# Performance work log

Hardware: AMD Instinct MI355X
Metric: run time of the kernel (lower is better)

## Reference

```python
import jax, jax.numpy as jnp
import numpy as np

WS = (8, 8)          # window size (Wh, Ww)
SS = (4, 4)          # shift size
DIM = 512
HEADS = 16
HD = DIM // HEADS    # 32
D1 = (HD // 2) // 2  # 8
D2 = (HD // 2) - D1  # 8
EPS = 1e-5
B, H, W = 4, 128, 128
HIDDEN = int(DIM * 4.0)  # 2048 (swiglu -> fc1 out = 2*HIDDEN)


def _layer_norm(x, g, b):
    m = jnp.mean(x, -1, keepdims=True)
    v = jnp.mean((x - m) ** 2, -1, keepdims=True)
    return (x - m) * jax.lax.rsqrt(v + EPS) * g + b


def _rope_tables():
    wh, ww = WS
    inv1 = 10000.0 ** (-(jnp.arange(D1, dtype=jnp.float32) / D1))
    inv2 = 10000.0 ** (-(jnp.arange(D2, dtype=jnp.float32) / D2))
    rows = jnp.arange(wh, dtype=jnp.float32)[:, None] * inv1  # (wh, D1)
    cols = jnp.arange(ww, dtype=jnp.float32)[:, None] * inv2  # (ww, D2)
    sin1 = jnp.broadcast_to(jnp.sin(rows)[:, None, :], (wh, ww, D1))
    cos1 = jnp.broadcast_to(jnp.cos(rows)[:, None, :], (wh, ww, D1))
    sin2 = jnp.broadcast_to(jnp.sin(cols)[None, :, :], (wh, ww, D2))
    cos2 = jnp.broadcast_to(jnp.cos(cols)[None, :, :], (wh, ww, D2))
    return sin1, cos1, sin2, cos2


def _rope2d(t, tabs):
    # t: (B_*heads, wh, ww, HD)
    sin1, cos1, sin2, cos2 = tabs
    x11 = t[..., :D1]
    x21 = t[..., D1:D1 + D2]
    x12 = t[..., D1 + D2:D1 + D2 + D1]
    x22 = t[..., D1 + D2 + D1:]
    return jnp.concatenate([
        x11 * cos1 - x12 * sin1,
        x21 * cos2 - x22 * sin2,
        x12 * cos1 + x11 * sin1,
        x22 * cos2 + x21 * sin2,
    ], axis=-1)


def _swin_mask():
    wh, ww = WS
    img = np.zeros((H, W), dtype=np.float32)
    cnt = 0
    for hs in (slice(0, -wh), slice(-wh, -SS[0]), slice(-SS[0], None)):
        for ws in (slice(0, -ww), slice(-ww, -SS[1]), slice(-SS[1], None)):
            img[hs, ws] = cnt
            cnt += 1
    mw = img.reshape(H // wh, wh, W // ww, ww).transpose(0, 2, 1, 3).reshape(-1, wh * ww)
    diff = mw[:, None, :] - mw[:, :, None]
    return jnp.asarray(np.where(diff != 0, -100.0, 0.0).astype(np.float32))


def setup_inputs() -> dict:
    key = jax.random.key(0)
    ks = jax.random.split(key, 14)
    s = 0.02
    return {
        "x": jax.random.normal(ks[0], (B, H, W, DIM), jnp.float32),
        "attn_mask": _swin_mask(),
        "norm1_g": jnp.ones((DIM,), jnp.float32),
        "norm1_b": jnp.zeros((DIM,), jnp.float32),
        "qkv_w": jax.random.normal(ks[1], (3 * DIM, DIM), jnp.float32) * s,
        "qkv_b": jnp.zeros((3 * DIM,), jnp.float32),
        "proj_w": jax.random.normal(ks[2], (DIM, DIM), jnp.float32) * s,
        "proj_b": jnp.zeros((DIM,), jnp.float32),
        "norm2_g": jnp.ones((DIM,), jnp.float32),
        "norm2_b": jnp.zeros((DIM,), jnp.float32),
        "fc1_w": jax.random.normal(ks[3], (2 * HIDDEN, DIM), jnp.float32) * s,
        "fc1_b": jnp.zeros((2 * HIDDEN,), jnp.float32),
        "fc2_w": jax.random.normal(ks[4], (DIM, HIDDEN), jnp.float32) * s,
        "fc2_b": jnp.zeros((DIM,), jnp.float32),
    }


def reference(x, attn_mask, norm1_g, norm1_b, qkv_w, qkv_b, proj_w, proj_b,
              norm2_g, norm2_b, fc1_w, fc1_b, fc2_w, fc2_b):
    wh, ww = WS
    N = wh * ww
    nH, nW = H // wh, W // ww
    nWin = nH * nW
    B_ = B * nWin
    tabs = _rope_tables()

    shortcut = x
    xn = _layer_norm(x, norm1_g, norm1_b)
    # cyclic shift
    xs = jnp.roll(xn, (-SS[0], -SS[1]), axis=(1, 2))
    # window partition: (B,H,W,C) -> (B*nWin, N, C)
    xw = xs.reshape(B, nH, wh, nW, ww, DIM).transpose(0, 1, 3, 2, 4, 5).reshape(B_, N, DIM)

    qkv = xw @ qkv_w.T + qkv_b
    qkv = qkv.reshape(B_, N, 3, HEADS, HD).transpose(2, 0, 3, 1, 4)  # (3,B_,h,N,hd)
    q, k, v = qkv[0], qkv[1], qkv[2]
    # inline 2D RoPE on q,k per window
    q = _rope2d(q.reshape(-1, wh, ww, HD), tabs).reshape(B_, HEADS, N, HD)
    k = _rope2d(k.reshape(-1, wh, ww, HD), tabs).reshape(B_, HEADS, N, HD)

    scale = HD ** -0.5
    attn = jnp.einsum('bhnd,bhmd->bhnm', q * scale, k)
    attn = attn.reshape(B, nWin, HEADS, N, N) + attn_mask[None, :, None]
    attn = jax.nn.softmax(attn.reshape(B_, HEADS, N, N), axis=-1)

    out = jnp.einsum('bhnm,bhmd->bhnd', attn, v).transpose(0, 2, 1, 3).reshape(B_, N, DIM)
    out = out @ proj_w.T + proj_b
    # window reverse + reverse shift
    out = out.reshape(B, nH, nW, wh, ww, DIM).transpose(0, 1, 3, 2, 4, 5).reshape(B, H, W, DIM)
    out = jnp.roll(out, (SS[0], SS[1]), axis=(1, 2))

    x = shortcut + out
    # SwiGLU MLP
    y = _layer_norm(x, norm2_g, norm2_b)
    h = y @ fc1_w.T + fc1_b
    a, gate = jnp.split(h, 2, axis=-1)
    h = jax.nn.silu(gate) * a
    y = h @ fc2_w.T + fc2_b
    return x + y
```

## Files before the change

kernel.cpp:

```cpp
#include <hip/hip_runtime.h>
#include <stdint.h>

typedef __attribute__((ext_vector_type(8))) short bf16x8;
typedef __attribute__((ext_vector_type(4))) float f32x4;
typedef __attribute__((ext_vector_type(4))) int i32x4;
typedef unsigned short u16;

#define GLD_LDS16(g, l) __builtin_amdgcn_global_load_lds( \
    (const __attribute__((address_space(1))) void*)(g),   \
    (__attribute__((address_space(3))) void*)(l), 16, 0, 0)

#define PB() do { __builtin_amdgcn_sched_barrier(0); \
                  __builtin_amdgcn_s_barrier();      \
                  __builtin_amdgcn_sched_barrier(0); } while (0)

#define ACCI(d, a_, b_)  d = __builtin_amdgcn_mfma_i32_16x16x64_i8(a_, b_, d, 0, 0, 0)

#define INV_A (1.0f / 16384.0f)
#define INV_P (1.0f / 32768.0f)
#define INV_H (1.0f / 65536.0f)

__device__ __forceinline__ u16 f2bf(float f) {
  union { float f; uint32_t u; } a; a.f = f;
  uint32_t u = a.u;
  return (u16)((u + 0x7fffu + ((u >> 16) & 1u)) >> 16);
}
__device__ __forceinline__ float bf2f(u16 h) {
  union { uint32_t u; float f; } a; a.u = ((uint32_t)h) << 16;
  return a.f;
}
__device__ __forceinline__ uint32_t q8x4(float a, float b, float c, float d, float s) {
  int qa = (int)rintf(fminf(fmaxf(a * s, -127.f), 127.f));
  int qb = (int)rintf(fminf(fmaxf(b * s, -127.f), 127.f));
  int qc = (int)rintf(fminf(fmaxf(c * s, -127.f), 127.f));
  int qd = (int)rintf(fminf(fmaxf(d * s, -127.f), 127.f));
  return (qa & 255) | ((qb & 255) << 8) | ((qc & 255) << 16) | ((qd & 255) << 24);
}
__device__ __forceinline__ char q8(float v, float s) {
  return (char)(int)rintf(fminf(fmaxf(v * s, -127.f), 127.f));
}

__global__ __launch_bounds__(256) void ln1_wconv(const float* __restrict__ x,
    const float* __restrict__ gw, const float* __restrict__ bw, char* __restrict__ out,
    const float* __restrict__ qw, const float* __restrict__ pw,
    const float* __restrict__ f1w, const float* __restrict__ f2w,
    char* __restrict__ wb8) {
  int bx = blockIdx.x;
  if (bx >= 16384) {
    int i4 = (bx - 16384) * 1024 + threadIdx.x * 4;
    float w[4];
#pragma unroll
    for (int j = 0; j < 4; j++) {
      int idx = i4 + j;
      if (idx < 786432)        w[j] = qw[idx];
      else if (idx < 1048576)  w[j] = pw[idx - 786432];
      else if (idx < 3145728)  w[j] = f1w[idx - 1048576];
      else                     w[j] = f2w[idx - 3145728];
    }
    *(uint32_t*)(wb8 + i4) = q8x4(w[0], w[1], w[2], w[3], 1024.f);
    return;
  }
  int wid = threadIdx.x >> 6;
  int lane = threadIdx.x & 63;
  int m = (bx << 2) + wid;
  int n = m & 63;
  int bwin = m >> 6;
  int b = bwin >> 8;
  int wi = bwin & 255;
  int h = (((wi >> 4) << 3) + (n >> 3) + 4) & 127;
  int w = (((wi & 15) << 3) + (n & 7) + 4) & 127;
  const float* src = x + (((size_t)((b << 7) + h) << 7) + (size_t)w) * 512;
  int ch = lane << 3;
  float4 v0 = *(const float4*)(src + ch);
  float4 v1 = *(const float4*)(src + ch + 4);
  float vv[8] = {v0.x, v0.y, v0.z, v0.w, v1.x, v1.y, v1.z, v1.w};
  float s = 0.f, s2 = 0.f;
#pragma unroll
  for (int j = 0; j < 8; j++) { s += vv[j]; s2 += vv[j] * vv[j]; }
#pragma unroll
  for (int off = 32; off; off >>= 1) {
    s += __shfl_xor(s, off);
    s2 += __shfl_xor(s2, off);
  }
  float mean = s * (1.f / 512.f);
  float var = s2 * (1.f / 512.f) - mean * mean;
  float rstd = rsqrtf(var + 1e-5f);
  float y[8];
#pragma unroll
  for (int j = 0; j < 8; j++) y[j] = (vv[j] - mean) * rstd * gw[ch + j] + bw[ch + j];
  uint2 o;
  o.x = q8x4(y[0], y[1], y[2], y[3], 16.f);
  o.y = q8x4(y[4], y[5], y[6], y[7], 16.f);
  *(uint2*)(out + ((size_t)m << 9) + ch) = o;
}

__global__ __launch_bounds__(256) void ln2_q8(const u16* __restrict__ sb,
    const float* __restrict__ gw, const float* __restrict__ bw,
    char* __restrict__ out) {
  int wid = threadIdx.x >> 6;
  int lane = threadIdx.x & 63;
  int m = (blockIdx.x << 2) + wid;
  int ch = lane << 3;
  union { uint4 u; u16 hh[8]; } in;
  in.u = *(const uint4*)(sb + ((size_t)m << 9) + ch);
  float vv[8];
#pragma unroll
  for (int j = 0; j < 8; j++) vv[j] = bf2f(in.hh[j]);
  float s = 0.f, s2 = 0.f;
#pragma unroll
  for (int j = 0; j < 8; j++) { s += vv[j]; s2 += vv[j] * vv[j]; }
#pragma unroll
  for (int off = 32; off; off >>= 1) {
    s += __shfl_xor(s, off);
    s2 += __shfl_xor(s2, off);
  }
  float mean = s * (1.f / 512.f);
  float var = s2 * (1.f / 512.f) - mean * mean;
  float rstd = rsqrtf(var + 1e-5f);
  float y[8];
#pragma unroll
  for (int j = 0; j < 8; j++) y[j] = (vv[j] - mean) * rstd * gw[ch + j] + bw[ch + j];
  uint2 o;
  o.x = q8x4(y[0], y[1], y[2], y[3], 16.f);
  o.y = q8x4(y[4], y[5], y[6], y[7], 16.f);
  *(uint2*)(out + ((size_t)m << 9) + ch) = o;
}

template<int EPI, int K>
__global__ __launch_bounds__(512, 4) void gemm2i(
    const char* __restrict__ A, const char* __restrict__ Bw,
    const float* __restrict__ bias, void* __restrict__ outp,
    const float* __restrict__ resid, int NTN) {
  __shared__ __align__(16) char lds[2][3][8192];
  const int NT = K / 64;
  int bid = blockIdx.x;
  int nwg = gridDim.x;
  int wg = (bid & 7) * (nwg >> 3) + (bid >> 3);
  int mt = wg / NTN, nt = wg - mt * NTN;
  int m0 = mt << 7;
  int n0 = (EPI == 3) ? (nt << 7) : (nt << 8);

  int tid = threadIdx.x;
  int wid = tid >> 6, lane = tid & 63;
  int wm = wid >> 2, wn = wid & 3;
  int l15 = lane & 15, lhi = lane >> 4;

  int sr0 = tid >> 2;
  int sc = (tid & 3) ^ ((sr0 >> 1) & 3);
  const char* gA  = A  + (size_t)(m0 + sr0) * K + sc * 16;
  const char* gB0 = Bw + (size_t)(n0 + sr0) * K + sc * 16;
  const char* gB1 = (EPI == 3)
      ? (Bw + (size_t)(2048 + n0 + sr0) * K + sc * 16)
      : (Bw + (size_t)(n0 + 128 + sr0) * K + sc * 16);

  auto stage = [&](int slot, const char* gp, int t) {
    if (t >= NT) return;
    char* ld = &lds[t & 1][slot][0] + tid * 16;
    GLD_LDS16(gp + t * 64, ld);
  };

  int aoff[4], boff[2];
#pragma unroll
  for (int i = 0; i < 4; i++) {
    int r = wm * 64 + i * 16 + l15;
    aoff[i] = r * 64 + ((lhi ^ ((r >> 1) & 3)) << 4);
  }
#pragma unroll
  for (int j = 0; j < 2; j++) {
    int r = wn * 32 + j * 16 + l15;
    boff[j] = r * 64 + ((lhi ^ ((r >> 1) & 3)) << 4);
  }

  i32x4 acc[2][4][2] = {};
  i32x4 afr[4], b0r[2], b1r[2];

  stage(0, gA, 0); stage(1, gB0, 0); stage(2, gB1, 0);
  stage(0, gA, 1); stage(1, gB0, 1);
  asm volatile("s_waitcnt vmcnt(2)" ::: "memory");
  __builtin_amdgcn_sched_barrier(0);
  __builtin_amdgcn_s_barrier();
  __builtin_amdgcn_sched_barrier(0);

  for (int s = 0; s < NT; ++s) {
    const char* Ah  = &lds[s & 1][0][0];
    const char* B0h = &lds[s & 1][1][0];
    const char* B1h = &lds[s & 1][2][0];

#pragma unroll
    for (int i = 0; i < 4; i++) afr[i] = *(const i32x4*)&Ah[aoff[i]];
#pragma unroll
    for (int j = 0; j < 2; j++) b0r[j] = *(const i32x4*)&B0h[boff[j]];
    stage(2, gB1, s + 1);
    PB();
    __builtin_amdgcn_s_setprio(1);
#pragma unroll
    for (int i = 0; i < 4; i++)
#pragma unroll
      for (int j = 0; j < 2; j++) ACCI(acc[0][i][j], afr[i], b0r[j]);
    __builtin_amdgcn_s_setprio(0);
    PB();

#pragma unroll
    for (int j = 0; j < 2; j++) b1r[j] = *(const i32x4*)&B1h[boff[j]];
    stage(0, gA, s + 2);
    stage(1, gB0, s + 2);
    PB();
    __builtin_amdgcn_s_setprio(1);
#pragma unroll
    for (int i = 0; i < 4; i++)
#pragma unroll
      for (int j = 0; j < 2; j++) ACCI(acc[1][i][j], afr[i], b1r[j]);
    __builtin_amdgcn_s_setprio(0);
    if (s >= NT - 2) { asm volatile("s_waitcnt vmcnt(0)" ::: "memory"); }
    else             { asm volatile("s_waitcnt vmcnt(2)" ::: "memory"); }
    __builtin_amdgcn_sched_barrier(0);
    __builtin_amdgcn_s_barrier();
    __builtin_amdgcn_sched_barrier(0);
  }

#pragma unroll
  for (int i = 0; i < 4; i++) {
    int row = m0 + wm * 64 + i * 16 + lhi * 4;
    if (EPI == 0) {
      u16* out = (u16*)outp;
#pragma unroll
      for (int h = 0; h < 2; h++)
#pragma unroll
        for (int j = 0; j < 2; j++) {
          int colb = n0 + h * 128 + wn * 32 + j * 16;
          int col = colb + l15;
          int sh = colb >> 5;
          int d = (colb & 31) + l15;
          float bv = bias[col];
#pragma unroll
          for (int rg = 0; rg < 4; rg++)
            out[(size_t)sh * 2097152 + (size_t)(row + rg) * 32 + d] =
                f2bf((float)acc[h][i][j][rg] * INV_A + bv);
        }
    } else if (EPI == 1) {
      u16* sbw = (u16*)outp;
#pragma unroll
      for (int rg = 0; rg < 4; rg++) {
        int m = row + rg;
        int b = m >> 14, wi2 = (m >> 6) & 255, n = m & 63;
        int hh = (((wi2 >> 4) << 3) + (n >> 3) + 4) & 127;
        int w = (((wi2 & 15) << 3) + (n & 7) + 4) & 127;
        size_t pix = (((size_t)((b << 7) + hh) << 7) + (size_t)w) << 9;
#pragma unroll
        for (int h = 0; h < 2; h++)
#pragma unroll
          for (int j = 0; j < 2; j++) {
            int col = n0 + h * 128 + wn * 32 + j * 16 + l15;
            sbw[pix + col] = f2bf(resid[pix + col] +
                                  (float)acc[h][i][j][rg] * INV_P + bias[col]);
          }
      }
    } else if (EPI == 2) {
      float* out = (float*)outp;
      const u16* sbp = (const u16*)resid;
#pragma unroll
      for (int h = 0; h < 2; h++)
#pragma unroll
        for (int j = 0; j < 2; j++) {
          int col = n0 + h * 128 + wn * 32 + j * 16 + l15;
          float bv = bias[col];
#pragma unroll
          for (int rg = 0; rg < 4; rg++) {
            size_t idx = (size_t)(row + rg) * 512 + col;
            out[idx] = bf2f(sbp[idx]) + (float)acc[h][i][j][rg] * INV_H + bv;
          }
        }
    } else {
      char* out = (char*)outp;
#pragma unroll
      for (int j = 0; j < 2; j++) {
        int col = n0 + wn * 32 + j * 16 + l15;
        float ba_ = bias[col], bg_ = bias[col + 2048];
#pragma unroll
        for (int rg = 0; rg < 4; rg++) {
          float av = (float)acc[0][i][j][rg] * INV_A + ba_;
          float gv = (float)acc[1][i][j][rg] * INV_A + bg_;
          float sw = gv / (1.f + __expf(-gv));
          out[(size_t)(row + rg) * 2048 + col] = q8(sw * av, 64.f);
        }
      }
    }
  }
}

__global__ __launch_bounds__(256) void attn_mfma(
    const u16* __restrict__ qkv, char* __restrict__ out) {
  __shared__ __align__(16) char alds[4][15360];
  int tid = threadIdx.x;
  int wid = tid >> 6, lane = tid & 63;
  int bwin = blockIdx.x >> 2;
  int head = ((blockIdx.x & 3) << 2) + wid;
  int wi = bwin & 255;
  int wr = wi >> 4, wc = wi & 15;
  char* Wb = alds[wid];
  u16* Qr = (u16*)Wb;
  u16* Kr = (u16*)(Wb + 5120);
  u16* Vt = (u16*)(Wb + 10240);
  u16* PT = (u16*)Wb;
  int t = lane;
  int l15 = lane & 15, lhi = lane >> 4;
  size_t tok = (size_t)(bwin << 6) + t;
  const u16* qb = qkv + (size_t)head * 2097152 + tok * 32;
  union U { uint4 u; u16 s[8]; };
  U vq[4], vk[4], vv[4];
#pragma unroll
  for (int g = 0; g < 4; g++) {
    vq[g].u = *(const uint4*)(qb + (g << 3));
    vk[g].u = *(const uint4*)(qb + 33554432 + (g << 3));
    vv[g].u = *(const uint4*)(qb + 67108864 + (g << 3));
  }
  float q[32], k[32];
#pragma unroll
  for (int j = 0; j < 32; j++) {
    q[j] = bf2f(vq[j >> 3].s[j & 7]);
    k[j] = bf2f(vk[j >> 3].s[j & 7]);
  }
  int r = t >> 3, c = t & 7;
#pragma unroll
  for (int d = 0; d < 16; d++) {
    float pos = (d < 8) ? (float)r : (float)c;
    int dd = (d < 8) ? d : d - 8;
    float ang = pos * __expf(-(float)dd * 1.1512925465f);
    float sn, cs;
    __sincosf(ang, &sn, &cs);
    float q1 = q[d], q2 = q[d + 16];
    q[d] = q1 * cs - q2 * sn;  q[d + 16] = q2 * cs + q1 * sn;
    float k1 = k[d], k2 = k[d + 16];
    k[d] = k1 * cs - k2 * sn;  k[d + 16] = k2 * cs + k1 * sn;
  }
#pragma unroll
  for (int j = 0; j < 32; j++) q[j] *= 0.17677669529663687f;
#pragma unroll
  for (int sl = 0; sl < 4; sl++) {
    U tq, tk;
#pragma unroll
    for (int j = 0; j < 8; j++) { tq.s[j] = f2bf(q[sl * 8 + j]); tk.s[j] = f2bf(k[sl * 8 + j]); }
    *(uint4*)(Qr + t * 40 + sl * 8) = tq.u;
    *(uint4*)(Kr + t * 40 + sl * 8) = tk.u;
  }
#pragma unroll
  for (int j = 0; j < 32; j++) Vt[j * 72 + t] = vv[j >> 3].s[j & 7];
  bf16x8 kf[4], qf[4];
#pragma unroll
  for (int i = 0; i < 4; i++) {
    kf[i] = *(const bf16x8*)(Kr + (i * 16 + l15) * 40 + lhi * 8);
    qf[i] = *(const bf16x8*)(Qr + (i * 16 + l15) * 40 + lhi * 8);
  }
  f32x4 zz = {0.f, 0.f, 0.f, 0.f};
  f32x4 st[4][4];
#pragma unroll
  for (int mi = 0; mi < 4; mi++)
#pragma unroll
    for (int nj = 0; nj < 4; nj++)
      st[mi][nj] = __builtin_amdgcn_mfma_f32_16x16x32_bf16(kf[mi], qf[nj], zz, 0, 0, 0);
  if (wr == 15 || wc == 15) {
    int idh = (wr == 15) ? ((r >= 4) ? 2 : 1) : 0;
    int idw = (wc == 15) ? ((c >= 4) ? 2 : 1) : 0;
    int code = idh * 3 + idw;
    int cq[4], cm[4][4];
#pragma unroll
    for (int nj = 0; nj < 4; nj++) cq[nj] = __shfl(code, nj * 16 + l15);
#pragma unroll
    for (int mi = 0; mi < 4; mi++)
#pragma unroll
      for (int rg = 0; rg < 4; rg++) cm[mi][rg] = __shfl(code, mi * 16 + lhi * 4 + rg);
#pragma unroll
    for (int mi = 0; mi < 4; mi++)
#pragma unroll
      for (int nj = 0; nj < 4; nj++)
#pragma unroll
        for (int rg = 0; rg < 4; rg++)
          if (cm[mi][rg] != cq[nj]) st[mi][nj][rg] -= 100.f;
  }
  float inv_[4];
#pragma unroll
  for (int nj = 0; nj < 4; nj++) {
    float mx = -1e30f;
#pragma unroll
    for (int mi = 0; mi < 4; mi++)
#pragma unroll
      for (int rg = 0; rg < 4; rg++) mx = fmaxf(mx, st[mi][nj][rg]);
    mx = fmaxf(mx, __shfl_xor(mx, 16));
    mx = fmaxf(mx, __shfl_xor(mx, 32));
    float sum = 0.f;
#pragma unroll
    for (int mi = 0; mi < 4; mi++)
#pragma unroll
      for (int rg = 0; rg < 4; rg++) {
        float p = __expf(st[mi][nj][rg] - mx);
        st[mi][nj][rg] = p;
        sum += p;
      }
    sum += __shfl_xor(sum, 16);
    sum += __shfl_xor(sum, 32);
    inv_[nj] = 1.f / sum;
  }
#pragma unroll
  for (int mi = 0; mi < 4; mi++)
#pragma unroll
    for (int nj = 0; nj < 4; nj++) {
      uint32_t lo, hi;
      asm("v_cvt_pk_bf16_f32 %0, %1, %2" : "=v"(lo) : "v"(st[mi][nj][0]), "v"(st[mi][nj][1]));
      asm("v_cvt_pk_bf16_f32 %0, %1, %2" : "=v"(hi) : "v"(st[mi][nj][2]), "v"(st[mi][nj][3]));
      uint2 pr; pr.x = lo; pr.y = hi;
      *(uint2*)(PT + (nj * 16 + l15) * 72 + mi * 16 + lhi * 4) = pr;
    }
  bf16x8 vf[2][2], pf[4][2];
#pragma unroll
  for (int i = 0; i < 2; i++)
#pragma unroll
    for (int kc = 0; kc < 2; kc++)
      vf[i][kc] = *(const bf16x8*)(Vt + (i * 16 + l15) * 72 + kc * 32 + lhi * 8);
#pragma unroll
  for (int nj = 0; nj < 4; nj++)
#pragma unroll
    for (int kc = 0; kc < 2; kc++)
      pf[nj][kc] = *(const bf16x8*)(PT + (nj * 16 + l15) * 72 + kc * 32 + lhi * 8);
  char* Ot = Wb;
#pragma unroll
  for (int i = 0; i < 2; i++)
#pragma unroll
    for (int nj = 0; nj < 4; nj++) {
      f32x4 o = __builtin_amdgcn_mfma_f32_16x16x32_bf16(vf[i][0], pf[nj][0], zz, 0, 0, 0);
      o = __builtin_amdgcn_mfma_f32_16x16x32_bf16(vf[i][1], pf[nj][1], o, 0, 0, 0);
      float iv32 = inv_[nj] * 32.f;
      uint32_t pk = q8x4(o[0] * iv32, o[1] * iv32, o[2] * iv32, o[3] * iv32, 1.f);
      *(uint32_t*)(Ot + (nj * 16 + l15) * 40 + i * 16 + lhi * 4) = pk;
    }
#pragma unroll
  for (int g = 0; g < 4; g++) {
    int tl = g * 16 + (lane >> 2);
    int ch_ = (lane & 3) << 3;
    uint2 v = *(const uint2*)(Ot + tl * 40 + ch_);
    *(uint2*)(out + (size_t)((bwin << 6) + tl) * 512 + (head << 5) + ch_) = v;
  }
}

extern "C" void kernel_launch(void* const* d_in, const int* in_sizes, int n_in,
                              void* d_out, int out_size, void* d_ws, size_t ws_size,
                              hipStream_t stream) {
  (void)in_sizes; (void)n_in; (void)out_size; (void)ws_size;
  const float* x      = (const float*)d_in[0];
  const float* n1g    = (const float*)d_in[2];
  const float* n1b    = (const float*)d_in[3];
  const float* qkv_w  = (const float*)d_in[4];
  const float* qkv_b  = (const float*)d_in[5];
  const float* proj_w = (const float*)d_in[6];
  const float* proj_b = (const float*)d_in[7];
  const float* n2g    = (const float*)d_in[8];
  const float* n2b    = (const float*)d_in[9];
  const float* fc1_w  = (const float*)d_in[10];
  const float* fc1_b  = (const float*)d_in[11];
  const float* fc2_w  = (const float*)d_in[12];
  const float* fc2_b  = (const float*)d_in[13];

  const size_t MB = 1048576ULL;
  char* ws = (char*)d_ws;
  char* wb8  = ws;
  char* wq8  = wb8;
  char* wp8  = wb8 + 786432;
  char* wf18 = wb8 + 1048576;
  char* wf28 = wb8 + 3145728;
  char* xw8  = ws + 8 * MB;
  char* attn8 = xw8;
  u16*  qkvb = (u16*)(ws + 72 * MB);
  char* hb8  = ws + 8 * MB;
  u16*  sb   = (u16*)(ws + 264 * MB);
  char* yb8  = ws + 328 * MB;

  ln1_wconv<<<20480, 256, 0, stream>>>(x, n1g, n1b, xw8,
                                       qkv_w, proj_w, fc1_w, fc2_w, wb8);
  gemm2i<0, 512><<<3072, 512, 0, stream>>>(xw8, wq8, qkv_b, qkvb, nullptr, 6);
  attn_mfma<<<4096, 256, 0, stream>>>(qkvb, attn8);
  gemm2i<1, 512><<<1024, 512, 0, stream>>>(attn8, wp8, proj_b, sb, x, 2);
  ln2_q8<<<16384, 256, 0, stream>>>(sb, n2g, n2b, yb8);
  gemm2i<3, 512><<<8192, 512, 0, stream>>>(yb8, wf18, fc1_b, hb8, nullptr, 16);
  gemm2i<2, 2048><<<1024, 512, 0, stream>>>(hb8, wf28, fc2_b, d_out,
                                            (const float*)sb, 2);
}
```

Baseline: 564.7 us.

## Fuse projection GEMM with residual add and LayerNorm2 into one kernel

Replaces the separate projection GEMM (with residual epilogue) and the standalone ln2_q8 kernel with a single proj_ln2 kernel. Each workgroup computes a full 128x512 row tile, so it can do the row statistics for LayerNorm in its epilogue. Partial sums are reduced with lane shuffles and then through LDS across waves. It then writes both the bf16 residual sum and the int8-quantized normalized output. This removes a kernel launch and a full re-read of the bf16 intermediate, at the cost of a larger per-block tile, one block per CU, and byte-granular scattered stores.

```diff
diff --git a/kernel.cpp b/kernel.cpp
--- a/kernel.cpp
+++ b/kernel.cpp
@@ -94,38 +94,6 @@
   *(uint2*)(out + ((size_t)m << 9) + ch) = o;
 }
 
-__global__ __launch_bounds__(256) void ln2_q8(const u16* __restrict__ sb,
-    const float* __restrict__ gw, const float* __restrict__ bw,
-    char* __restrict__ out) {
-  int wid = threadIdx.x >> 6;
-  int lane = threadIdx.x & 63;
-  int m = (blockIdx.x << 2) + wid;
-  int ch = lane << 3;
-  union { uint4 u; u16 hh[8]; } in;
-  in.u = *(const uint4*)(sb + ((size_t)m << 9) + ch);
-  float vv[8];
-#pragma unroll
-  for (int j = 0; j < 8; j++) vv[j] = bf2f(in.hh[j]);
-  float s = 0.f, s2 = 0.f;
-#pragma unroll
-  for (int j = 0; j < 8; j++) { s += vv[j]; s2 += vv[j] * vv[j]; }
-#pragma unroll
-  for (int off = 32; off; off >>= 1) {
-    s += __shfl_xor(s, off);
-    s2 += __shfl_xor(s2, off);
-  }
-  float mean = s * (1.f / 512.f);
-  float var = s2 * (1.f / 512.f) - mean * mean;
-  float rstd = rsqrtf(var + 1e-5f);
-  float y[8];
-#pragma unroll
-  for (int j = 0; j < 8; j++) y[j] = (vv[j] - mean) * rstd * gw[ch + j] + bw[ch + j];
-  uint2 o;
-  o.x = q8x4(y[0], y[1], y[2], y[3], 16.f);
-  o.y = q8x4(y[4], y[5], y[6], y[7], 16.f);
-  *(uint2*)(out + ((size_t)m << 9) + ch) = o;
-}
-
 template<int EPI, int K>
 __global__ __launch_bounds__(512, 4) void gemm2i(
     const char* __restrict__ A, const char* __restrict__ Bw,
@@ -237,24 +205,6 @@
             out[(size_t)sh * 2097152 + (size_t)(row + rg) * 32 + d] =
                 f2bf((float)acc[h][i][j][rg] * INV_A + bv);
         }
-    } else if (EPI == 1) {
-      u16* sbw = (u16*)outp;
-#pragma unroll
-      for (int rg = 0; rg < 4; rg++) {
-        int m = row + rg;
-        int b = m >> 14, wi2 = (m >> 6) & 255, n = m & 63;
-        int hh = (((wi2 >> 4) << 3) + (n >> 3) + 4) & 127;
-        int w = (((wi2 & 15) << 3) + (n & 7) + 4) & 127;
-        size_t pix = (((size_t)((b << 7) + hh) << 7) + (size_t)w) << 9;
-#pragma unroll
-        for (int h = 0; h < 2; h++)
-#pragma unroll
-          for (int j = 0; j < 2; j++) {
-            int col = n0 + h * 128 + wn * 32 + j * 16 + l15;
-            sbw[pix + col] = f2bf(resid[pix + col] +
-                                  (float)acc[h][i][j][rg] * INV_P + bias[col]);
-          }
-      }
     } else if (EPI == 2) {
       float* out = (float*)outp;
       const u16* sbp = (const u16*)resid;
@@ -286,6 +236,172 @@
       }
     }
   }
+}
+
+__global__ __launch_bounds__(512, 1) void proj_ln2(
+    const char* __restrict__ A, const char* __restrict__ Bw,
+    const float* __restrict__ pbias, const float* __restrict__ g2,
+    const float* __restrict__ b2, const float* __restrict__ xres,
+    u16* __restrict__ sbw, char* __restrict__ yb8) {
+  __shared__ __align__(16) char lds[2][40960];
+  const int K = 512, NT = 8;
+  int bid = blockIdx.x;
+  int nwg = gridDim.x;
+  int wg = (bid & 7) * (nwg >> 3) + (bid >> 3);
+  int m0 = wg << 7;
+
+  int tid = threadIdx.x;
+  int wid = tid >> 6, lane = tid & 63;
+  int wm = wid >> 2, wn = wid & 3;
+  int l15 = lane & 15, lhi = lane >> 4;
+
+  int sr0 = tid >> 2;
+  int sc = (tid & 3) ^ ((sr0 >> 1) & 3);
+  const char* gA = A + (size_t)(m0 + sr0) * K + sc * 16;
+  const char* gB[4];
+#pragma unroll
+  for (int q = 0; q < 4; q++)
+    gB[q] = Bw + (size_t)(q * 128 + sr0) * K + sc * 16;
+
+  auto stageA = [&](int t) {
+    if (t >= NT) return;
+    GLD_LDS16(gA + t * 64, &lds[t & 1][0] + tid * 16);
+  };
+  auto stageB = [&](int q, int t) {
+    if (t >= NT) return;
+    GLD_LDS16(gB[q] + t * 64, &lds[t & 1][8192 + q * 8192] + tid * 16);
+  };
+
+  int aoff[4], boff[8];
+#pragma unroll
+  for (int i = 0; i < 4; i++) {
+    int r = wm * 64 + i * 16 + l15;
+    aoff[i] = r * 64 + ((lhi ^ ((r >> 1) & 3)) << 4);
+  }
+#pragma unroll
+  for (int j = 0; j < 8; j++) {
+    int r = wn * 128 + j * 16 + l15;
+    boff[j] = 8192 + r * 64 + ((lhi ^ ((r >> 1) & 3)) << 4);
+  }
+
+  i32x4 acc[4][8] = {};
+  i32x4 afr[4], br[4];
+
+  stageA(0); stageB(0, 0); stageB(1, 0); stageB(2, 0); stageB(3, 0);
+  stageA(1);
+  asm volatile("s_waitcnt vmcnt(1)" ::: "memory");
+  __builtin_amdgcn_sched_barrier(0);
+  __builtin_amdgcn_s_barrier();
+  __builtin_amdgcn_sched_barrier(0);
+
+  for (int s = 0; s < NT; ++s) {
+    const char* Lh = &lds[s & 1][0];
+
+#pragma unroll
+    for (int i = 0; i < 4; i++) afr[i] = *(const i32x4*)&Lh[aoff[i]];
+#pragma unroll
+    for (int j = 0; j < 4; j++) br[j] = *(const i32x4*)&Lh[boff[j]];
+    stageB(0, s + 1); stageB(1, s + 1); stageB(2, s + 1); stageB(3, s + 1);
+    PB();
+    __builtin_amdgcn_s_setprio(1);
+#pragma unroll
+    for (int i = 0; i < 4; i++)
+#pragma unroll
+      for (int j = 0; j < 4; j++) ACCI(acc[i][j], afr[i], br[j]);
+    __builtin_amdgcn_s_setprio(0);
+    PB();
+
+#pragma unroll
+    for (int j = 0; j < 4; j++) br[j] = *(const i32x4*)&Lh[boff[4 + j]];
+    stageA(s + 2);
+    PB();
+    __builtin_amdgcn_s_setprio(1);
+#pragma unroll
+    for (int i = 0; i < 4; i++)
+#pragma unroll
+      for (int j = 0; j < 4; j++) ACCI(acc[i][4 + j], afr[i], br[j]);
+    __builtin_amdgcn_s_setprio(0);
+    if (s >= NT - 2) { asm volatile("s_waitcnt vmcnt(0)" ::: "memory"); }
+    else             { asm volatile("s_waitcnt vmcnt(1)" ::: "memory"); }
+    __builtin_amdgcn_sched_barrier(0);
+    __builtin_amdgcn_s_barrier();
+    __builtin_amdgcn_sched_barrier(0);
+  }
+
+  float pb_[8], gv_[8], bv_[8];
+#pragma unroll
+  for (int j = 0; j < 8; j++) {
+    int col = wn * 128 + j * 16 + l15;
+    pb_[j] = pbias[col];
+    gv_[j] = g2[col];
+    bv_[j] = b2[col];
+  }
+  size_t pix[4][4];
+  float s1[4][4], s2_[4][4];
+#pragma unroll
+  for (int i = 0; i < 4; i++)
+#pragma unroll
+    for (int rg = 0; rg < 4; rg++) {
+      int m = m0 + wm * 64 + i * 16 + lhi * 4 + rg;
+      int b = m >> 14, wi2 = (m >> 6) & 255, n = m & 63;
+      int hh = (((wi2 >> 4) << 3) + (n >> 3) + 4) & 127;
+      int w = (((wi2 & 15) << 3) + (n & 7) + 4) & 127;
+      pix[i][rg] = (((size_t)((b << 7) + hh) << 7) + (size_t)w) << 9;
+      float a1 = 0.f, a2 = 0.f;
+#pragma unroll
+      for (int j = 0; j < 8; j++) {
+        int col = wn * 128 + j * 16 + l15;
+        float sv = xres[pix[i][rg] + col] + (float)acc[i][j][rg] * INV_P + pb_[j];
+        sbw[pix[i][rg] + col] = f2bf(sv);
+        acc[i][j][rg] = __float_as_int(sv);
+        a1 += sv; a2 += sv * sv;
+      }
+      s1[i][rg] = a1; s2_[i][rg] = a2;
+    }
+#pragma unroll
+  for (int i = 0; i < 4; i++)
+#pragma unroll
+    for (int rg = 0; rg < 4; rg++) {
+#pragma unroll
+      for (int off = 1; off < 16; off <<= 1) {
+        s1[i][rg] += __shfl_xor(s1[i][rg], off);
+        s2_[i][rg] += __shfl_xor(s2_[i][rg], off);
+      }
+    }
+  float* st = (float*)lds;
+  __syncthreads();
+  if (l15 == 0) {
+#pragma unroll
+    for (int i = 0; i < 4; i++)
+#pragma unroll
+      for (int rg = 0; rg < 4; rg++) {
+        int lrow = wm * 64 + i * 16 + lhi * 4 + rg;
+        st[(lrow * 4 + wn) * 2]     = s1[i][rg];
+        st[(lrow * 4 + wn) * 2 + 1] = s2_[i][rg];
+      }
+  }
+  __syncthreads();
+#pragma unroll
+  for (int i = 0; i < 4; i++)
+#pragma unroll
+    for (int rg = 0; rg < 4; rg++) {
+      int lrow = wm * 64 + i * 16 + lhi * 4 + rg;
+      float m1 = 0.f, m2 = 0.f;
+#pragma unroll
+      for (int w4 = 0; w4 < 4; w4++) {
+        m1 += st[(lrow * 4 + w4) * 2];
+        m2 += st[(lrow * 4 + w4) * 2 + 1];
+      }
+      float mean = m1 * (1.f / 512.f);
+      float var = m2 * (1.f / 512.f) - mean * mean;
+      float rstd = rsqrtf(var + 1e-5f);
+#pragma unroll
+      for (int j = 0; j < 8; j++) {
+        int col = wn * 128 + j * 16 + l15;
+        float y = (__int_as_float(acc[i][j][rg]) - mean) * rstd * gv_[j] + bv_[j];
+        yb8[pix[i][rg] + col] = q8(y, 16.f);
+      }
+    }
 }
 
 __global__ __launch_bounds__(256) void attn_mfma(
@@ -477,8 +593,7 @@
                                        qkv_w, proj_w, fc1_w, fc2_w, wb8);
   gemm2i<0, 512><<<3072, 512, 0, stream>>>(xw8, wq8, qkv_b, qkvb, nullptr, 6);
   attn_mfma<<<4096, 256, 0, stream>>>(qkvb, attn8);
-  gemm2i<1, 512><<<1024, 512, 0, stream>>>(attn8, wp8, proj_b, sb, x, 2);
-  ln2_q8<<<16384, 256, 0, stream>>>(sb, n2g, n2b, yb8);
+  proj_ln2<<<512, 512, 0, stream>>>(attn8, wp8, proj_b, n2g, n2b, x, sb, yb8);
   gemm2i<3, 512><<<8192, 512, 0, stream>>>(yb8, wf18, fc1_b, hb8, nullptr, 16);
   gemm2i<2, 2048><<<1024, 512, 0, stream>>>(hb8, wf28, fc2_b, d_out,
                                             (const float*)sb, 2);
```

Result: slower. 622.9 us (+10.3%).
